# Kernel optimization log

Measured on AMD Instinct MI355X. Metric: run time of the kernel, lower is better.

The kernel has to match this reference:

```python
import jax, jax.numpy as jnp
import numpy as np


def _mlp(x, W0, b0, W1, b1, W2, b2, W3, b3):
    # 4-layer MLP, ReLU between layers, no final activation
    h = jax.nn.relu(x @ W0 + b0)
    h = jax.nn.relu(h @ W1 + b1)
    h = jax.nn.relu(h @ W2 + b2)
    return h @ W3 + b3


def setup_inputs() -> dict:
    key = jax.random.key(0)
    ks = jax.random.split(key, 8)
    B, t, p, f = 4, 12, 32, 64          # num_graphs, timesteps, n_patches, nhid
    n = 10000                            # nodes per graph
    E = 200000                           # subgraph-node membership entries
    in_dim = f * t + t                   # 780
    horizon = 12
    scale = 0.02
    return {
        "mixer_x": jax.random.normal(ks[0], (B, t, p, f), jnp.float32),
        "features": jax.random.normal(ks[1], (B * n, t), jnp.float32),
        "subgraphs_batch": jax.random.randint(ks[2], (E,), 0, p * B),
        "subgraphs_nodes_mapper": jax.random.randint(ks[3], (E,), 0, n * B),
        "W0": jax.random.normal(ks[4], (in_dim, in_dim), jnp.float32) * scale,
        "b0": jnp.zeros((in_dim,), jnp.float32),
        "W1": jax.random.normal(ks[5], (in_dim, in_dim), jnp.float32) * scale,
        "b1": jnp.zeros((in_dim,), jnp.float32),
        "W2": jax.random.normal(ks[6], (in_dim, in_dim), jnp.float32) * scale,
        "b2": jnp.zeros((in_dim,), jnp.float32),
        "W3": jax.random.normal(ks[7], (in_dim, horizon), jnp.float32) * scale,
        "b3": jnp.zeros((horizon,), jnp.float32),
    }


def reference(mixer_x, features, subgraphs_batch, subgraphs_nodes_mapper,
              W0, b0, W1, b1, W2, b2, W3, b3):
    B, t, p, f = mixer_x.shape
    n_seg = features.shape[0]                      # n * B segments
    n = n_seg // B
    # passthrough: '(B n) t -> B n t'
    passthrough = features.reshape(B, n, t)
    # mixer_x: 'B t p f -> (p B) t f'
    flat = jnp.transpose(mixer_x, (2, 0, 1, 3)).reshape(p * B, t, f)
    # gather by subgraph index, then scatter-mean over node mapper
    gathered = flat[subgraphs_batch]               # (E, t, f)
    sums = jax.ops.segment_sum(gathered, subgraphs_nodes_mapper, num_segments=n_seg)
    counts = jax.ops.segment_sum(jnp.ones((gathered.shape[0],), gathered.dtype),
                                 subgraphs_nodes_mapper, num_segments=n_seg)
    nodes = sums / jnp.maximum(counts, 1.0)[:, None, None]   # (n*B, t, f)
    # '(n B) t f -> B n (t f)'
    nodes = jnp.transpose(nodes.reshape(n, B, t, f), (1, 0, 2, 3)).reshape(B, n, t * f)
    mlp_in = jnp.concatenate([passthrough, nodes], axis=-1)  # (B, n, t + t*f)
    mlp_out = _mlp(mlp_in, W0, b0, W1, b1, W2, b2, W3, b3)   # (B, n, horizon)
    # 'B n h -> (B n) h'
    return mlp_out.reshape(B * n, -1)
```

## Files before the change

kernel.cpp:

```cpp
#include <hip/hip_runtime.h>

#define BG    4
#define TT    12
#define NN    10000
#define EN    200000
#define NSEG  40000
#define NROWS 40000
#define MPAD  40064
#define KD    832
#define KA0   160
#define NPW   896
#define NT    7

typedef __attribute__((ext_vector_type(8))) short bf8_t;
typedef __attribute__((ext_vector_type(4))) float f4_t;

__device__ __forceinline__ unsigned short f2bf(float x) {
  unsigned int u = __float_as_uint(x);
  u += 0x7fffu + ((u >> 16) & 1u);
  return (unsigned short)(u >> 16);
}

#define GLDS16(src, dst) __builtin_amdgcn_global_load_lds( \
    (const __attribute__((address_space(1))) void*)(src),  \
    (__attribute__((address_space(3))) void*)(dst), 16, 0, 0)

__global__ void k_zero(int* counts) {
  int i = blockIdx.x * 256 + threadIdx.x;
  if (i < NSEG) counts[i] = 0;
}

__global__ void k_count(const int* __restrict__ mapper, int* __restrict__ counts) {
  int e = blockIdx.x * 256 + threadIdx.x;
  if (e < EN) atomicAdd(&counts[mapper[e]], 1);
}

__global__ void k_zerof(float* __restrict__ p, int n) {
  int i = blockIdx.x * 256 + threadIdx.x;
  if (i < n) p[i] = 0.f;
}

__global__ void k_scatterCf(const int* __restrict__ mapper, const int* __restrict__ batch,
                            float* __restrict__ Cff) {
  int e = blockIdx.x * 256 + threadIdx.x;
  if (e < EN) {
    const int s = mapper[e];
    const int r = (s % BG) * NN + s / BG;
    atomicAdd(&Cff[(size_t)r * 128 + batch[e]], 1.0f);
  }
}

__global__ void k_buildA(const float* __restrict__ features, const int* __restrict__ counts,
                         const float* __restrict__ Cff, unsigned short* __restrict__ A) {
  int idx = blockIdx.x * 256 + threadIdx.x;
  if (idx >= MPAD * KA0) return;
  const int r = idx / KA0, c = idx - r * KA0;
  float v = 0.f;
  if (r < NROWS) {
    if (c < 12) {
      v = features[(size_t)r * TT + c];
    } else if (c < 140) {
      const int s = (r % NN) * BG + (r / NN);
      const int cnt = counts[s];
      const float inv = 1.f / (float)(cnt > 0 ? cnt : 1);
      v = Cff[(size_t)r * 128 + (c - 12)] * inv;
    }
  }
  A[idx] = f2bf(v);
}

__global__ void k_buildB(const float* __restrict__ W0, const float* __restrict__ fW0,
                         unsigned short* __restrict__ WTB) {
  int idx = blockIdx.x * 256 + threadIdx.x;
  if (idx >= NPW * KA0) return;
  const int n = idx / KA0, k = idx - n * KA0;
  float v = 0.f;
  if (n < 780) {
    if (k < 12) v = W0[(size_t)k * 780 + n];
    else if (k < 140) v = fW0[(size_t)(k - 12) * KD + n];
  }
  WTB[idx] = f2bf(v);
}

__global__ void k_tpad(const float* __restrict__ W, unsigned short* __restrict__ Wt,
                       int ldw, int nsrc, int total) {
  int idx = blockIdx.x * 256 + threadIdx.x;
  if (idx >= total) return;
  int n = idx / KD, k = idx % KD;
  float v = (n < nsrc && k < 780) ? W[k * ldw + n] : 0.f;
  Wt[idx] = f2bf(v);
}

__global__ void k_padbias3(const float* __restrict__ b0, const float* __restrict__ b1,
                           const float* __restrict__ b2, float* __restrict__ p0,
                           float* __restrict__ p1, float* __restrict__ p2) {
  int i = blockIdx.x * 256 + threadIdx.x;
  if (i >= 3 * KD) return;
  const int which = i / KD, c = i - which * KD;
  const float* src = which == 0 ? b0 : (which == 1 ? b1 : b2);
  float* dst = which == 0 ? p0 : (which == 1 ? p1 : p2);
  dst[c] = (c < 780) ? src[c] : 0.f;
}

__global__ __launch_bounds__(256) void k_flatW0(const float* __restrict__ mixer,
                                                const float* __restrict__ W0,
                                                float* __restrict__ fW0) {
  __shared__ float sA[8][768];
  __shared__ float sRed[4][64][9];
  const int tid = threadIdx.x;
  const int c0 = blockIdx.x * 64, j0 = blockIdx.y * 8;
  for (int i = tid; i < 8 * 768; i += 256) {
    int jj = i / 768;
    int k = i - jj * 768;
    int j = j0 + jj;
    int tt = k >> 6, ff = k & 63;
    sA[jj][k] = mixer[(((j & 3) * TT + tt) * 32 + (j >> 2)) * 64 + ff];
  }
  __syncthreads();
  const int cc = tid & 63, ks = tid >> 6;
  const int c = c0 + cc;
  float acc[8] = {};
  if (c < 780) {
    const float* wp = W0 + (size_t)(12 + ks * 192) * 780 + c;
    #pragma unroll 4
    for (int k = ks * 192; k < ks * 192 + 192; ++k) {
      const float w = *wp; wp += 780;
      #pragma unroll
      for (int jj = 0; jj < 8; ++jj) acc[jj] = fmaf(sA[jj][k], w, acc[jj]);
    }
  }
  #pragma unroll
  for (int jj = 0; jj < 8; ++jj) sRed[ks][cc][jj] = acc[jj];
  __syncthreads();
  for (int o = tid; o < 512; o += 256) {
    const int oc = o & 63, jj = o >> 6;
    const int wc = c0 + oc;
    if (wc < KD) {
      float s = sRed[0][oc][jj] + sRed[1][oc][jj] + sRed[2][oc][jj] + sRed[3][oc][jj];
      fW0[(size_t)(j0 + jj) * KD + wc] = s;
    }
  }
}

template<int KA, int BK>
__global__ __launch_bounds__(256) void gemm_relu(
    const unsigned short* __restrict__ A, const unsigned short* __restrict__ WT,
    const float* __restrict__ bias, unsigned short* __restrict__ C) {
  constexpr int SEGR = BK / 8;
  constexpr int NISS = (128 * SEGR) / 256;
  __shared__ unsigned short sA[128 * BK];
  __shared__ unsigned short sB[128 * BK];
  const int tid = threadIdx.x, lane = tid & 63, wid = tid >> 6;
  const int wm = wid >> 1, wn = wid & 1;

  const int nwg = gridDim.x;
  const int q = nwg >> 3, r8 = nwg & 7;
  const int xcd = blockIdx.x & 7, bidx = blockIdx.x >> 3;
  const int linear = (xcd < r8 ? xcd * (q + 1) : r8 * (q + 1) + (xcd - r8) * q) + bidx;
  const int rowtile = linear / NT, ntile = linear - rowtile * NT;

  const int row0 = rowtile * 128, n0 = ntile * 128;
  const char* gA = (const char*)A + (size_t)row0 * (KA * 2);
  const char* gB = (const char*)WT + (size_t)n0 * (KA * 2);
  const int frow = lane & 15, fk = (lane >> 4) * 8;

  f4_t acc[4][4] = {};

  for (int kt = 0; kt < KA / BK; ++kt) {
    const int kb = kt * (BK * 2);
    __syncthreads();
    #pragma unroll
    for (int L = 0; L < NISS; ++L) {
      const int seg = L * 256 + wid * 64 + lane;
      const int row = seg / SEGR, c16 = seg & (SEGR - 1);
      const size_t go = (size_t)row * (KA * 2) + kb + c16 * 16;
      GLDS16(gA + go, (char*)sA + seg * 16);
      GLDS16(gB + go, (char*)sB + seg * 16);
    }
    __syncthreads();
    #pragma unroll
    for (int kk = 0; kk < BK / 32; ++kk) {
      bf8_t af[4], bfr[4];
      #pragma unroll
      for (int mi = 0; mi < 4; ++mi)
        af[mi] = *(const bf8_t*)(&sA[(wm * 64 + mi * 16 + frow) * BK + kk * 32 + fk]);
      #pragma unroll
      for (int ni = 0; ni < 4; ++ni)
        bfr[ni] = *(const bf8_t*)(&sB[(wn * 64 + ni * 16 + frow) * BK + kk * 32 + fk]);
      #pragma unroll
      for (int mi = 0; mi < 4; ++mi)
        #pragma unroll
        for (int ni = 0; ni < 4; ++ni)
          acc[mi][ni] = __builtin_amdgcn_mfma_f32_16x16x32_bf16(bfr[ni], af[mi], acc[mi][ni], 0, 0, 0);
    }
  }

  const int cq = (lane >> 4) * 4;
  #pragma unroll
  for (int mi = 0; mi < 4; ++mi) {
    const int r = row0 + wm * 64 + mi * 16 + frow;
    unsigned short* crow = C + (size_t)r * KD;
    #pragma unroll
    for (int ni = 0; ni < 4; ++ni) {
      const int c = n0 + wn * 64 + ni * 16 + cq;
      if (c < KD) {
        f4_t v = acc[mi][ni];
        const f4_t bb = *(const f4_t*)(bias + c);
        float v0 = fmaxf(v[0] + bb[0], 0.f);
        float v1 = fmaxf(v[1] + bb[1], 0.f);
        float v2 = fmaxf(v[2] + bb[2], 0.f);
        float v3 = fmaxf(v[3] + bb[3], 0.f);
        uint2 pk;
        pk.x = (unsigned int)f2bf(v0) | ((unsigned int)f2bf(v1) << 16);
        pk.y = (unsigned int)f2bf(v2) | ((unsigned int)f2bf(v3) << 16);
        *(uint2*)(crow + c) = pk;
      }
    }
  }
}

__global__ __launch_bounds__(256) void gemm_out(
    const unsigned short* __restrict__ A, const unsigned short* __restrict__ WT3,
    const float* __restrict__ b3, float* __restrict__ out) {
  __shared__ unsigned short sA[128 * 64];
  __shared__ unsigned short sB[16 * 64];
  const int tid = threadIdx.x, lane = tid & 63, wid = tid >> 6;
  const int row0 = blockIdx.x * 128;
  const char* gA = (const char*)A + (size_t)row0 * (KD * 2);
  const char* gB = (const char*)WT3;
  const int frow = lane & 15, fk = (lane >> 4) * 8;

  f4_t acc[2] = {};

  for (int kt = 0; kt < KD / 64; ++kt) {
    const int kb = kt * 128;
    __syncthreads();
    #pragma unroll
    for (int L = 0; L < 4; ++L) {
      const int seg = L * 256 + wid * 64 + lane;
      const int row = seg >> 3, c16 = seg & 7;
      GLDS16(gA + (size_t)row * (KD * 2) + kb + c16 * 16, (char*)sA + seg * 16);
    }
    if (wid == 0) {
      #pragma unroll
      for (int L = 0; L < 2; ++L) {
        const int seg = L * 64 + lane;
        const int row = seg >> 3, c16 = seg & 7;
        GLDS16(gB + (size_t)row * (KD * 2) + kb + c16 * 16, (char*)sB + seg * 16);
      }
    }
    __syncthreads();
    #pragma unroll
    for (int kk = 0; kk < 2; ++kk) {
      const bf8_t bf = *(const bf8_t*)(&sB[frow * 64 + kk * 32 + fk]);
      #pragma unroll
      for (int mi = 0; mi < 2; ++mi) {
        const bf8_t af = *(const bf8_t*)(&sA[(wid * 32 + mi * 16 + frow) * 64 + kk * 32 + fk]);
        acc[mi] = __builtin_amdgcn_mfma_f32_16x16x32_bf16(bf, af, acc[mi], 0, 0, 0);
      }
    }
  }

  const int cg = (lane >> 4) * 4;
  #pragma unroll
  for (int mi = 0; mi < 2; ++mi) {
    const int r = row0 + wid * 32 + mi * 16 + frow;
    if (r < NROWS && cg < 12) {
      f4_t v = acc[mi];
      const f4_t bb = *(const f4_t*)(b3 + cg);
      v += bb;
      *(f4_t*)(out + (size_t)r * 12 + cg) = v;
    }
  }
}

extern "C" void kernel_launch(void* const* d_in, const int* in_sizes, int n_in,
                              void* d_out, int out_size, void* d_ws, size_t ws_size,
                              hipStream_t stream) {
  const float* mixer    = (const float*)d_in[0];
  const float* features = (const float*)d_in[1];
  const int*   sg_batch = (const int*)d_in[2];
  const int*   sg_map   = (const int*)d_in[3];
  const float* W0 = (const float*)d_in[4];  const float* b0 = (const float*)d_in[5];
  const float* W1 = (const float*)d_in[6];  const float* b1 = (const float*)d_in[7];
  const float* W2 = (const float*)d_in[8];  const float* b2 = (const float*)d_in[9];
  const float* W3 = (const float*)d_in[10]; const float* b3 = (const float*)d_in[11];
  float* out = (float*)d_out;

  char* wsp = (char*)d_ws;
  auto alloc = [&](size_t bytes) { char* p = wsp; wsp += (bytes + 255) & ~(size_t)255; return p; };
  unsigned short* h0  = (unsigned short*)alloc((size_t)MPAD * KD * 2);
  unsigned short* h1  = (unsigned short*)alloc((size_t)MPAD * KD * 2);
  unsigned short* Wt1 = (unsigned short*)alloc((size_t)NPW * KD * 2);
  unsigned short* Wt2 = (unsigned short*)alloc((size_t)NPW * KD * 2);
  unsigned short* Wt3 = (unsigned short*)alloc((size_t)16 * KD * 2);
  unsigned short* WTB = (unsigned short*)alloc((size_t)NPW * KA0 * 2);
  float* bp0   = (float*)alloc(KD * 4);
  float* bp1   = (float*)alloc(KD * 4);
  float* bp2   = (float*)alloc(KD * 4);
  float* fW0   = (float*)alloc((size_t)128 * KD * 4);
  int* counts  = (int*)alloc(NSEG * 4);
  float* Cff = (float*)h1;
  unsigned short* Abuf = (unsigned short*)((char*)h1 + ((size_t)MPAD * 128 * 4 + 255 & ~(size_t)255));

  k_zero<<<(NSEG + 255) / 256, 256, 0, stream>>>(counts);
  k_count<<<(EN + 255) / 256, 256, 0, stream>>>(sg_map, counts);

  k_zerof<<<(MPAD * 128 + 255) / 256, 256, 0, stream>>>(Cff, MPAD * 128);
  k_scatterCf<<<(EN + 255) / 256, 256, 0, stream>>>(sg_map, sg_batch, Cff);

  k_flatW0<<<dim3(13, 16), 256, 0, stream>>>(mixer, W0, fW0);
  k_tpad<<<(NPW * KD + 255) / 256, 256, 0, stream>>>(W1, Wt1, 780, 780, NPW * KD);
  k_tpad<<<(NPW * KD + 255) / 256, 256, 0, stream>>>(W2, Wt2, 780, 780, NPW * KD);
  k_tpad<<<(16 * KD + 255) / 256, 256, 0, stream>>>(W3, Wt3, 12, 12, 16 * KD);
  k_padbias3<<<(3 * KD + 255) / 256, 256, 0, stream>>>(b0, b1, b2, bp0, bp1, bp2);
  k_buildB<<<(NPW * KA0 + 255) / 256, 256, 0, stream>>>(W0, fW0, WTB);

  k_buildA<<<(MPAD * KA0 + 255) / 256, 256, 0, stream>>>(features, counts, Cff, Abuf);

  gemm_relu<KA0, 32><<<(MPAD / 128) * NT, 256, 0, stream>>>(Abuf, WTB, bp0, h0);

  gemm_relu<KD, 64><<<(MPAD / 128) * NT, 256, 0, stream>>>(h0, Wt1, bp1, h1);
  gemm_relu<KD, 64><<<(MPAD / 128) * NT, 256, 0, stream>>>(h1, Wt2, bp2, h0);

  gemm_out<<<MPAD / 128, 256, 0, stream>>>(h0, Wt3, b3, out);
}
```

Before: 375.8 us.

## Double-buffer GEMM LDS tiles with swizzled layout and manual waitcnt pipelining

Rewrites the bf16 MFMA GEMM main loop to use two LDS buffers, prefetching tile t+2 while computing tile t, with hand-placed vmcnt/lgkmcnt waits and raw barriers in place of __syncthreads. LDS is laid out with an XOR swizzle on 16-byte chunks to cut bank conflicts on fragment reads, and fragment offsets are precomputed. It also raises wave priority around the MFMA block. The cost is twice the LDS use, which may lower occupancy, and fragile hand-tuned wait counts.

Result: faster. 359.9 us (-4.2%).

```diff
diff --git a/kernel.cpp b/kernel.cpp
--- a/kernel.cpp
+++ b/kernel.cpp
@@ -24,6 +24,9 @@
 #define GLDS16(src, dst) __builtin_amdgcn_global_load_lds( \
     (const __attribute__((address_space(1))) void*)(src),  \
     (__attribute__((address_space(3))) void*)(dst), 16, 0, 0)
+
+#define LKW0 asm volatile("s_waitcnt lgkmcnt(0)" ::: "memory")
+#define VMW0 asm volatile("s_waitcnt vmcnt(0)" ::: "memory")
 
 __global__ void k_zero(int* counts) {
   int i = blockIdx.x * 256 + threadIdx.x;
@@ -147,9 +150,12 @@
     const unsigned short* __restrict__ A, const unsigned short* __restrict__ WT,
     const float* __restrict__ bias, unsigned short* __restrict__ C) {
   constexpr int SEGR = BK / 8;
+  constexpr int MASK = SEGR - 1;
   constexpr int NISS = (128 * SEGR) / 256;
-  __shared__ unsigned short sA[128 * BK];
-  __shared__ unsigned short sB[128 * BK];
+  constexpr int NKT  = KA / BK;
+  constexpr int NKK  = BK / 32;
+  __shared__ unsigned short sA[2][128 * BK];
+  __shared__ unsigned short sB[2][128 * BK];
   const int tid = threadIdx.x, lane = tid & 63, wid = tid >> 6;
   const int wm = wid >> 1, wn = wid & 1;
 
@@ -162,36 +168,77 @@
   const int row0 = rowtile * 128, n0 = ntile * 128;
   const char* gA = (const char*)A + (size_t)row0 * (KA * 2);
   const char* gB = (const char*)WT + (size_t)n0 * (KA * 2);
-  const int frow = lane & 15, fk = (lane >> 4) * 8;
-
-  f4_t acc[4][4] = {};
-
-  for (int kt = 0; kt < KA / BK; ++kt) {
+  const int frow = lane & 15;
+
+  int offA[NKK][4], offB[NKK][4];
+  #pragma unroll
+  for (int kk = 0; kk < NKK; ++kk) {
+    const int c16r = kk * 4 + (lane >> 4);
+    #pragma unroll
+    for (int i = 0; i < 4; ++i) {
+      const int ra = wm * 64 + i * 16 + frow;
+      const int rb = wn * 64 + i * 16 + frow;
+      offA[kk][i] = ra * BK + ((c16r ^ (ra & MASK)) * 8);
+      offB[kk][i] = rb * BK + ((c16r ^ (rb & MASK)) * 8);
+    }
+  }
+
+  auto stage = [&](int b, int kt) {
     const int kb = kt * (BK * 2);
-    __syncthreads();
     #pragma unroll
     for (int L = 0; L < NISS; ++L) {
       const int seg = L * 256 + wid * 64 + lane;
-      const int row = seg / SEGR, c16 = seg & (SEGR - 1);
-      const size_t go = (size_t)row * (KA * 2) + kb + c16 * 16;
-      GLDS16(gA + go, (char*)sA + seg * 16);
-      GLDS16(gB + go, (char*)sB + seg * 16);
-    }
-    __syncthreads();
-    #pragma unroll
-    for (int kk = 0; kk < BK / 32; ++kk) {
-      bf8_t af[4], bfr[4];
-      #pragma unroll
-      for (int mi = 0; mi < 4; ++mi)
-        af[mi] = *(const bf8_t*)(&sA[(wm * 64 + mi * 16 + frow) * BK + kk * 32 + fk]);
-      #pragma unroll
-      for (int ni = 0; ni < 4; ++ni)
-        bfr[ni] = *(const bf8_t*)(&sB[(wn * 64 + ni * 16 + frow) * BK + kk * 32 + fk]);
+      const int row = seg / SEGR, c16 = seg & MASK;
+      const int c16s = c16 ^ (row & MASK);
+      const size_t go = (size_t)row * (KA * 2) + kb + c16s * 16;
+      GLDS16(gA + go, (char*)sA[b] + seg * 16);
+      GLDS16(gB + go, (char*)sB[b] + seg * 16);
+    }
+  };
+
+  f4_t acc[4][4] = {};
+
+  stage(0, 0);
+  stage(1, 1);
+  if constexpr (BK == 64) asm volatile("s_waitcnt vmcnt(8)" ::: "memory");
+  else                    asm volatile("s_waitcnt vmcnt(4)" ::: "memory");
+  __builtin_amdgcn_s_barrier();
+
+  #pragma unroll
+  for (int t = 0; t < NKT; ++t) {
+    const int cur = t & 1;
+    bf8_t af[NKK][4], bfv[NKK][4];
+    #pragma unroll
+    for (int kk = 0; kk < NKK; ++kk) {
+      #pragma unroll
+      for (int i = 0; i < 4; ++i) {
+        af[kk][i]  = *(const bf8_t*)(&sA[cur][offA[kk][i]]);
+        bfv[kk][i] = *(const bf8_t*)(&sB[cur][offB[kk][i]]);
+      }
+    }
+    if (t < NKT - 1) {
+      LKW0;
+      __builtin_amdgcn_s_barrier();
+      __builtin_amdgcn_sched_barrier(0);
+      if (t + 2 < NKT) stage(cur, t + 2);
+    }
+    __builtin_amdgcn_s_setprio(1);
+    #pragma unroll
+    for (int kk = 0; kk < NKK; ++kk)
       #pragma unroll
       for (int mi = 0; mi < 4; ++mi)
         #pragma unroll
         for (int ni = 0; ni < 4; ++ni)
-          acc[mi][ni] = __builtin_amdgcn_mfma_f32_16x16x32_bf16(bfr[ni], af[mi], acc[mi][ni], 0, 0, 0);
+          acc[mi][ni] = __builtin_amdgcn_mfma_f32_16x16x32_bf16(bfv[kk][ni], af[kk][mi], acc[mi][ni], 0, 0, 0);
+    __builtin_amdgcn_s_setprio(0);
+    if (t < NKT - 1) {
+      if (t + 2 < NKT) {
+        if constexpr (BK == 64) asm volatile("s_waitcnt vmcnt(8)" ::: "memory");
+        else                    asm volatile("s_waitcnt vmcnt(4)" ::: "memory");
+      } else {
+        VMW0;
+      }
+      __builtin_amdgcn_s_barrier();
     }
   }
 
```
